# Kernel optimization log

Measured on AMD Instinct MI355X. Metric: run time of the kernel, lower is better.

## Reference

```python
import jax, jax.numpy as jnp
import numpy as np
from jax import lax

TOPK = 5
NUM_CLUSTERS = 10
MAX_ITERS = 10


def setup_inputs() -> dict:
    key = jax.random.key(0)
    k1, k2, k3 = jax.random.split(key, 3)
    B, S, D, K = 8, 4096, 256, 1024
    x = jax.random.normal(k1, (B, S, D), dtype=jnp.float32)
    memory = jax.random.normal(k2, (K, D), dtype=jnp.float32)
    init_idx = jax.random.randint(k3, (B, NUM_CLUSTERS), 0, S, dtype=jnp.int32)
    return {"x": x, "memory": memory, "init_idx": init_idx}


def reference(x, memory, init_idx):
    B, S, D = x.shape
    # --- memory bank retrieval ---
    sim = jnp.einsum('bsd,kd->bsk', x, memory)            # [B,S,K]
    _, topk_idx = lax.top_k(sim, TOPK)                    # [B,S,TOPK]
    memory_ctx = memory[topk_idx]                         # [B,S,TOPK,D]
    attn = jax.nn.softmax(jnp.einsum('bsd,bstd->bst', x, memory_ctx), axis=-1)
    x_enh = x + jnp.einsum('bst,bstd->bsd', attn, memory_ctx)  # [B,S,D]

    # --- in-place k-means ---
    centroids0 = jnp.take_along_axis(x_enh, init_idx[:, :, None], axis=1)  # [B,k,D]
    x_norm_sq = jnp.sum(x_enh ** 2, axis=-1, keepdims=True)                # [B,S,1]

    def step(cent, _):
        dots = jnp.einsum('bsd,bkd->bsk', x_enh, cent)                     # [B,S,k]
        c_norm_sq = jnp.sum(cent ** 2, axis=-1)                            # [B,k]
        dist = x_norm_sq - 2.0 * dots + c_norm_sq[:, None, :]              # [B,S,k]
        assign = jnp.argmin(dist, axis=-1)                                 # [B,S]
        onehot = jax.nn.one_hot(assign, NUM_CLUSTERS, dtype=x_enh.dtype)   # [B,S,k]
        sums = jnp.einsum('bsk,bsd->bkd', onehot, x_enh)                   # [B,k,D]
        counts = jnp.sum(onehot, axis=1)[:, :, None]                       # [B,k,1]
        new_cent = sums / (counts + 1e-8)
        return new_cent, assign

    cent, assigns = lax.scan(step, centroids0, None, length=MAX_ITERS)
    assign = assigns[-1]  # assignments from last iteration (pre final update, as in torch)
    idx = jnp.broadcast_to(assign[:, :, None], (B, S, D))
    quantized = jnp.take_along_axis(cent, idx, axis=1)  # [B,S,D]
    return quantized
```

## Files before the change

kernel.cpp:

```cpp
#include <hip/hip_runtime.h>
#include <math.h>

#define NC 10
#define KITERS 10

#define SWZ(row, q) ((q) ^ (((row) >> 2) & 15))

extern __shared__ float4 lds4[];
__global__ __launch_bounds__(256, 1) void k_enh(const float* __restrict__ x,
                                                const float* __restrict__ mem,
                                                float* __restrict__ xenh) {
  float4* xt = lds4;
  float4* mt = lds4 + 4096;
  float* cv = (float*)lds4;
  int*   ck = (int*)lds4 + 5120;
  float* av = (float*)lds4 + 10240;
  int*   ak = (int*)lds4 + 10560;

  const int tid = threadIdx.x;
  const int tg = tid >> 4;
  const int kg = tid & 15;
  const int tokenBase = blockIdx.x * 64;

  {
    const float4* xg = (const float4*)(x + (size_t)tokenBase * 256);
    const float4* mg = (const float4*)mem;
#pragma unroll
    for (int i = 0; i < 16; ++i) {
      const int p = tid + 256 * i;
      const int row = p >> 6, q = p & 63;
      xt[row * 64 + SWZ(row, q)] = xg[p];
      mt[row * 64 + SWZ(row, q)] = mg[p];
    }
  }
  __syncthreads();

  float t5v[4][5]; int t5k[4][5];
#pragma unroll
  for (int i = 0; i < 4; ++i)
#pragma unroll
    for (int r = 0; r < 5; ++r) { t5v[i][r] = -INFINITY; t5k[i][r] = 0; }

  for (int kc = 0; kc < 16; ++kc) {
    float4 st[16];
    if (kc < 15) {
      const float4* mg = (const float4*)mem + (size_t)(kc + 1) * 4096;
#pragma unroll
      for (int i = 0; i < 16; ++i) st[i] = mg[tid + 256 * i];
    }

    float4 acc[4][4];
#pragma unroll
    for (int i = 0; i < 4; ++i)
#pragma unroll
      for (int j = 0; j < 4; ++j) acc[i][j] = make_float4(0.f, 0.f, 0.f, 0.f);

#pragma unroll 8
    for (int q = 0; q < 64; ++q) {
      float4 mv[4], xv[4];
#pragma unroll
      for (int j = 0; j < 4; ++j) {
        const int row = 4 * kg + j;
        mv[j] = mt[row * 64 + SWZ(row, q)];
      }
#pragma unroll
      for (int i = 0; i < 4; ++i) {
        const int row = 4 * tg + i;
        xv[i] = xt[row * 64 + SWZ(row, q)];
      }
#pragma unroll
      for (int i = 0; i < 4; ++i)
#pragma unroll
        for (int j = 0; j < 4; ++j) {
          acc[i][j].x = __fadd_rn(acc[i][j].x, __fmul_rn(xv[i].x, mv[j].x));
          acc[i][j].y = __fadd_rn(acc[i][j].y, __fmul_rn(xv[i].y, mv[j].y));
          acc[i][j].z = __fadd_rn(acc[i][j].z, __fmul_rn(xv[i].z, mv[j].z));
          acc[i][j].w = __fadd_rn(acc[i][j].w, __fmul_rn(xv[i].w, mv[j].w));
        }
    }

#pragma unroll
    for (int i = 0; i < 4; ++i)
#pragma unroll
      for (int j = 0; j < 4; ++j) {
        const float v = __fadd_rn(__fadd_rn(acc[i][j].x, acc[i][j].z),
                                  __fadd_rn(acc[i][j].y, acc[i][j].w));
        const int kk = kc * 64 + 4 * kg + j;
        if (v > t5v[i][4]) {
          t5v[i][4] = v; t5k[i][4] = kk;
          if (t5v[i][4] > t5v[i][3]) { float a = t5v[i][3]; t5v[i][3] = t5v[i][4]; t5v[i][4] = a; int ia = t5k[i][3]; t5k[i][3] = t5k[i][4]; t5k[i][4] = ia; }
          if (t5v[i][3] > t5v[i][2]) { float a = t5v[i][2]; t5v[i][2] = t5v[i][3]; t5v[i][3] = a; int ia = t5k[i][2]; t5k[i][2] = t5k[i][3]; t5k[i][3] = ia; }
          if (t5v[i][2] > t5v[i][1]) { float a = t5v[i][1]; t5v[i][1] = t5v[i][2]; t5v[i][2] = a; int ia = t5k[i][1]; t5k[i][1] = t5k[i][2]; t5k[i][2] = ia; }
          if (t5v[i][1] > t5v[i][0]) { float a = t5v[i][0]; t5v[i][0] = t5v[i][1]; t5v[i][1] = a; int ia = t5k[i][0]; t5k[i][0] = t5k[i][1]; t5k[i][1] = ia; }
        }
      }

    __syncthreads();
    if (kc < 15) {
#pragma unroll
      for (int i = 0; i < 16; ++i) {
        const int p = tid + 256 * i;
        const int row = p >> 6, q = p & 63;
        mt[row * 64 + SWZ(row, q)] = st[i];
      }
      __syncthreads();
    }
  }
  __syncthreads();

#pragma unroll
  for (int i = 0; i < 4; ++i) {
    const int token = 4 * tg + i;
#pragma unroll
    for (int r = 0; r < 5; ++r) {
      cv[token * 80 + kg * 5 + r] = t5v[i][r];
      ck[token * 80 + kg * 5 + r] = t5k[i][r];
    }
  }
  __syncthreads();

  if (tid < 64) {
    const int token = tid;
    float tv[5]; int tk[5];
#pragma unroll
    for (int r = 0; r < 5; ++r) {
      float best = -INFINITY; int bi = 0, bk = 0x7fffffff;
      for (int c = 0; c < 80; ++c) {
        const float vv = cv[token * 80 + c]; const int kkc = ck[token * 80 + c];
        if (vv > best || (vv == best && kkc < bk)) { best = vv; bi = c; bk = kkc; }
      }
      tv[r] = best; tk[r] = bk; cv[token * 80 + bi] = -INFINITY;
    }
    float mx = tv[0];
#pragma unroll
    for (int r = 1; r < 5; ++r) mx = fmaxf(mx, tv[r]);
    float e[5];
#pragma unroll
    for (int r = 0; r < 5; ++r)
      e[r] = (float)exp((double)__fsub_rn(tv[r], mx));
    float s = e[0];
#pragma unroll
    for (int r = 1; r < 5; ++r) s = __fadd_rn(s, e[r]);
#pragma unroll
    for (int r = 0; r < 5; ++r) { av[token * 5 + r] = __fdiv_rn(e[r], s); ak[token * 5 + r] = tk[r]; }
  }
  __syncthreads();

#pragma unroll
  for (int i = 0; i < 16; ++i) {
    const int flat = tid + 256 * i;
    const int token = flat >> 6, q = flat & 63;
    const float a0 = av[token * 5 + 0], a1 = av[token * 5 + 1], a2 = av[token * 5 + 2],
                a3 = av[token * 5 + 3], a4 = av[token * 5 + 4];
    const float4 xv = ((const float4*)(x + (size_t)(tokenBase + token) * 256))[q];
    const float4 m0 = ((const float4*)(mem + (size_t)ak[token * 5 + 0] * 256))[q];
    const float4 m1 = ((const float4*)(mem + (size_t)ak[token * 5 + 1] * 256))[q];
    const float4 m2 = ((const float4*)(mem + (size_t)ak[token * 5 + 2] * 256))[q];
    const float4 m3 = ((const float4*)(mem + (size_t)ak[token * 5 + 3] * 256))[q];
    const float4 m4 = ((const float4*)(mem + (size_t)ak[token * 5 + 4] * 256))[q];
    float4 o;
    {
      float ctx = __fmul_rn(a0, m0.x);
      ctx = __fadd_rn(ctx, __fmul_rn(a1, m1.x));
      ctx = __fadd_rn(ctx, __fmul_rn(a2, m2.x));
      ctx = __fadd_rn(ctx, __fmul_rn(a3, m3.x));
      ctx = __fadd_rn(ctx, __fmul_rn(a4, m4.x));
      o.x = __fadd_rn(xv.x, ctx);
    }
    {
      float ctx = __fmul_rn(a0, m0.y);
      ctx = __fadd_rn(ctx, __fmul_rn(a1, m1.y));
      ctx = __fadd_rn(ctx, __fmul_rn(a2, m2.y));
      ctx = __fadd_rn(ctx, __fmul_rn(a3, m3.y));
      ctx = __fadd_rn(ctx, __fmul_rn(a4, m4.y));
      o.y = __fadd_rn(xv.y, ctx);
    }
    {
      float ctx = __fmul_rn(a0, m0.z);
      ctx = __fadd_rn(ctx, __fmul_rn(a1, m1.z));
      ctx = __fadd_rn(ctx, __fmul_rn(a2, m2.z));
      ctx = __fadd_rn(ctx, __fmul_rn(a3, m3.z));
      ctx = __fadd_rn(ctx, __fmul_rn(a4, m4.z));
      o.z = __fadd_rn(xv.z, ctx);
    }
    {
      float ctx = __fmul_rn(a0, m0.w);
      ctx = __fadd_rn(ctx, __fmul_rn(a1, m1.w));
      ctx = __fadd_rn(ctx, __fmul_rn(a2, m2.w));
      ctx = __fadd_rn(ctx, __fmul_rn(a3, m3.w));
      ctx = __fadd_rn(ctx, __fmul_rn(a4, m4.w));
      o.w = __fadd_rn(xv.w, ctx);
    }
    ((float4*)(xenh + (size_t)tokenBase * 256))[flat] = o;
  }
}

__global__ __launch_bounds__(256) void k_transpose_x(const float* __restrict__ in,
                                                     float* __restrict__ outT) {
  __shared__ float t[32][33];
  const int tx = threadIdx.x & 31, ty = threadIdx.x >> 5;
  const int s0 = blockIdx.x * 32, d0 = blockIdx.y * 32, b = blockIdx.z;
  const float* ib = in + (size_t)b * 4096 * 256;
  float* ob = outT + (size_t)b * 256 * 4096;
#pragma unroll
  for (int i = 0; i < 4; ++i)
    t[ty + 8 * i][tx] = ib[(size_t)(s0 + ty + 8 * i) * 256 + d0 + tx];
  __syncthreads();
#pragma unroll
  for (int i = 0; i < 4; ++i)
    ob[(size_t)(d0 + ty + 8 * i) * 4096 + s0 + tx] = t[tx][ty + 8 * i];
}

__global__ __launch_bounds__(256) void k_zero(int* __restrict__ p, int n) {
  const int i = blockIdx.x * 256 + threadIdx.x;
  if (i < n) p[i] = 0;
}

__global__ __launch_bounds__(64) void k_init(const float* __restrict__ xenh,
                                             const int* __restrict__ init_idx,
                                             float* __restrict__ cent) {
  const int i = blockIdx.x;
  const int b = i / NC;
  const int s = init_idx[i];
  const int l = threadIdx.x;
  ((float4*)(cent + (size_t)i * 256))[l] =
      ((const float4*)(xenh + ((size_t)b * 4096 + s) * 256))[l];
}

__global__ __launch_bounds__(256) void k_assign(const float* __restrict__ xenh,
                                                const float* __restrict__ cent,
                                                int* __restrict__ assign,
                                                int* __restrict__ cnt) {
  __shared__ float cl[NC * 256];
  const int tid = threadIdx.x;
  const int b = blockIdx.x & 7;
  const int j = blockIdx.x >> 3;
  const int tokenBase = b * 4096 + j * 128;
  for (int i = tid; i < NC * 256; i += 256)
    cl[i] = cent[(size_t)b * NC * 256 + i];
  __syncthreads();

  const int token = tokenBase + (tid >> 1);
  const int h = tid & 1;
  const float4* px4 = (const float4*)(xenh + (size_t)token * 256 + h * 128);
  const float* pc = cl + h * 128;

  float r[NC][8];
  float4 c0 = px4[0], c1 = px4[1];
#pragma unroll
  for (int ib = 0; ib < 16; ++ib) {
    float4 n0, n1;
    if (ib < 15) { n0 = px4[2 * ib + 2]; n1 = px4[2 * ib + 3]; }
    const float p8[8] = {c0.x, c0.y, c0.z, c0.w, c1.x, c1.y, c1.z, c1.w};
    const int i = ib * 8;
    if (ib == 0) {
#pragma unroll
      for (int k = 0; k < NC; ++k)
#pragma unroll
        for (int jj = 0; jj < 8; ++jj) {
          const float d = __fsub_rn(p8[jj], pc[k * 256 + jj]);
          r[k][jj] = __fmul_rn(d, d);
        }
    } else {
#pragma unroll
      for (int k = 0; k < NC; ++k)
#pragma unroll
        for (int jj = 0; jj < 8; ++jj) {
          const float d = __fsub_rn(p8[jj], pc[k * 256 + i + jj]);
          r[k][jj] = __fadd_rn(r[k][jj], __fmul_rn(d, d));
        }
    }
    c0 = n0; c1 = n1;
  }

  float best = INFINITY; int bk = 0;
#pragma unroll
  for (int k = 0; k < NC; ++k) {
    const float blkOwn =
        __fadd_rn(__fadd_rn(__fadd_rn(r[k][0], r[k][1]), __fadd_rn(r[k][2], r[k][3])),
                  __fadd_rn(__fadd_rn(r[k][4], r[k][5]), __fadd_rn(r[k][6], r[k][7])));
    const float blkOther = __shfl_xor(blkOwn, 1);
    const float dist = __fadd_rn(blkOwn, blkOther);
    if (dist < best) { best = dist; bk = k; }
  }
  if (h == 0) assign[token] = bk;
#pragma unroll
  for (int k = 0; k < NC; ++k) {
    const unsigned long long m =
        __ballot(bk == k) & 0x5555555555555555ULL;
    if ((tid & 63) == 0) atomicAdd(&cnt[b * NC + k], (int)__popcll(m));
  }
}

__global__ __launch_bounds__(64) void k_sums_T(const float* __restrict__ xT,
                                               const int* __restrict__ assign,
                                               const int* __restrict__ cnt,
                                               float* __restrict__ cent) {
  const int b = blockIdx.x & 7;
  const int rem = blockIdx.x >> 3;
  const int k = rem >> 2;
  const int d = (rem & 3) * 64 + threadIdx.x;
  const float4* xc = (const float4*)(xT + ((size_t)b * 256 + d) * 4096);
  const int4* ac = (const int4*)(assign + b * 4096);

  float acc = 0.0f;
  for (int c = 0; c < 64; ++c) {
    float4 xe[16]; int4 ar[16];
#pragma unroll
    for (int j = 0; j < 16; ++j) xe[j] = xc[c * 16 + j];
#pragma unroll
    for (int j = 0; j < 16; ++j) ar[j] = ac[c * 16 + j];
#pragma unroll
    for (int j = 0; j < 16; ++j) {
      acc = __fadd_rn(acc, (ar[j].x == k) ? xe[j].x : 0.0f);
      acc = __fadd_rn(acc, (ar[j].y == k) ? xe[j].y : 0.0f);
      acc = __fadd_rn(acc, (ar[j].z == k) ? xe[j].z : 0.0f);
      acc = __fadd_rn(acc, (ar[j].w == k) ? xe[j].w : 0.0f);
    }
  }
  const int cc = cnt[b * NC + k];
  cent[((size_t)(b * NC + k)) * 256 + d] = (cc == 0) ? 0.0f : __fdiv_rn(acc, (float)cc);
}

__global__ __launch_bounds__(64) void k_sums(const float* __restrict__ xenh,
                                             const int* __restrict__ assign,
                                             const int* __restrict__ cnt,
                                             float* __restrict__ cent) {
  const int b = blockIdx.x & 7;
  const int rem = blockIdx.x >> 3;
  const int k = rem >> 2;
  const int d = (rem & 3) * 64 + threadIdx.x;
  const float* xb = xenh + (size_t)b * 4096 * 256 + d;
  const int* ab = assign + b * 4096;

  float acc = 0.0f;
  for (int c = 0; c < 64; ++c) {
    float xe[64]; int ar[64];
#pragma unroll
    for (int j = 0; j < 64; ++j) xe[j] = xb[(size_t)(c * 64 + j) * 256];
#pragma unroll
    for (int j = 0; j < 64; ++j) ar[j] = ab[c * 64 + j];
#pragma unroll
    for (int j = 0; j < 64; ++j)
      acc = __fadd_rn(acc, (ar[j] == k) ? xe[j] : 0.0f);
  }
  const int cc = cnt[b * NC + k];
  cent[((size_t)(b * NC + k)) * 256 + d] = (cc == 0) ? 0.0f : __fdiv_rn(acc, (float)cc);
}

__global__ __launch_bounds__(256) void k_quant(const float* __restrict__ cent,
                                               const int* __restrict__ assign,
                                               float* __restrict__ out) {
  const int token = blockIdx.x * 4 + (threadIdx.x >> 6);
  const int l = threadIdx.x & 63;
  const int b = token >> 12;
  const int a = assign[token];
  ((float4*)out)[(size_t)token * 64 + l] =
      ((const float4*)cent)[(size_t)(b * NC + a) * 64 + l];
}

extern "C" void kernel_launch(void* const* d_in, const int* in_sizes, int n_in,
                              void* d_out, int out_size, void* d_ws, size_t ws_size,
                              hipStream_t stream) {
  const float* x = (const float*)d_in[0];
  const float* mem = (const float*)d_in[1];
  const int* init_idx = (const int*)d_in[2];
  float* xenh = (float*)d_out;
  char* ws = (char*)d_ws;

  float* cent   = (float*)(ws);
  int*   assign = (int*)  (ws + 81920);
  int*   cntbuf = (int*)  (ws + 212992);
  float* xT     = (float*)(ws + (1 << 20));
  const bool useT = ws_size >= ((size_t)34 << 20);

  (void)hipFuncSetAttribute((const void*)k_enh,
                            hipFuncAttributeMaxDynamicSharedMemorySize, 131072);

  k_zero<<<4, 256, 0, stream>>>(cntbuf, KITERS * 8 * NC);
  k_enh<<<512, 256, 131072, stream>>>(x, mem, xenh);
  if (useT) k_transpose_x<<<dim3(128, 8, 8), 256, 0, stream>>>(xenh, xT);
  k_init<<<80, 64, 0, stream>>>(xenh, init_idx, cent);
  for (int it = 0; it < KITERS; ++it) {
    k_assign<<<256, 256, 0, stream>>>(xenh, cent, assign, cntbuf + it * 8 * NC);
    if (useT)
      k_sums_T<<<320, 64, 0, stream>>>(xT, assign, cntbuf + it * 8 * NC, cent);
    else
      k_sums<<<320, 64, 0, stream>>>(xenh, assign, cntbuf + it * 8 * NC, cent);
  }
  k_quant<<<8192, 256, 0, stream>>>(cent, assign, (float*)d_out);
}
```

Baseline: 1.779 ms.

## Stage token tile in padded LDS and split each token across four lanes in assign

The k-means assignment kernel now loads a 64-token tile of x_enh into padded shared memory with coalesced float4 reads, then has four lanes per token compute partial distances that are combined with two shuffles. The grid doubles to 512 blocks and occupancy is set to two blocks per CU. This is meant to raise parallelism and memory coalescing over the old two-lanes-per-token version, which streamed x directly from global memory. In exchange it uses much more LDS per block and issues scalar LDS reads, which may be bank-conflict or LDS-bandwidth bound.

```diff
diff --git a/kernel.cpp b/kernel.cpp
--- a/kernel.cpp
+++ b/kernel.cpp
@@ -7,6 +7,7 @@
 #define SWZ(row, q) ((q) ^ (((row) >> 2) & 15))
 
 extern __shared__ float4 lds4[];
+
 __global__ __launch_bounds__(256, 1) void k_enh(const float* __restrict__ x,
                                                 const float* __restrict__ mem,
                                                 float* __restrict__ xenh) {
@@ -227,67 +228,71 @@
       ((const float4*)(xenh + ((size_t)b * 4096 + s) * 256))[l];
 }
 
-__global__ __launch_bounds__(256) void k_assign(const float* __restrict__ xenh,
-                                                const float* __restrict__ cent,
-                                                int* __restrict__ assign,
-                                                int* __restrict__ cnt) {
-  __shared__ float cl[NC * 256];
+__global__ __launch_bounds__(256, 2) void k_assign(const float* __restrict__ xenh,
+                                                   const float* __restrict__ cent,
+                                                   int* __restrict__ assign,
+                                                   int* __restrict__ cnt) {
+  float* xls = (float*)lds4;
+  float* cl  = (float*)lds4 + 64 * 257;
   const int tid = threadIdx.x;
   const int b = blockIdx.x & 7;
   const int j = blockIdx.x >> 3;
-  const int tokenBase = b * 4096 + j * 128;
+  const int tokenBase = b * 4096 + j * 64;
+
   for (int i = tid; i < NC * 256; i += 256)
     cl[i] = cent[(size_t)b * NC * 256 + i];
-  __syncthreads();
-
-  const int token = tokenBase + (tid >> 1);
-  const int h = tid & 1;
-  const float4* px4 = (const float4*)(xenh + (size_t)token * 256 + h * 128);
-  const float* pc = cl + h * 128;
-
-  float r[NC][8];
-  float4 c0 = px4[0], c1 = px4[1];
-#pragma unroll
-  for (int ib = 0; ib < 16; ++ib) {
-    float4 n0, n1;
-    if (ib < 15) { n0 = px4[2 * ib + 2]; n1 = px4[2 * ib + 3]; }
-    const float p8[8] = {c0.x, c0.y, c0.z, c0.w, c1.x, c1.y, c1.z, c1.w};
-    const int i = ib * 8;
-    if (ib == 0) {
-#pragma unroll
-      for (int k = 0; k < NC; ++k)
-#pragma unroll
-        for (int jj = 0; jj < 8; ++jj) {
-          const float d = __fsub_rn(p8[jj], pc[k * 256 + jj]);
-          r[k][jj] = __fmul_rn(d, d);
-        }
-    } else {
-#pragma unroll
-      for (int k = 0; k < NC; ++k)
-#pragma unroll
-        for (int jj = 0; jj < 8; ++jj) {
-          const float d = __fsub_rn(p8[jj], pc[k * 256 + i + jj]);
-          r[k][jj] = __fadd_rn(r[k][jj], __fmul_rn(d, d));
-        }
-    }
-    c0 = n0; c1 = n1;
-  }
+  {
+    const float4* xg = (const float4*)(xenh + (size_t)tokenBase * 256);
+#pragma unroll
+    for (int i = 0; i < 16; ++i) {
+      const int f = tid + 256 * i;
+      const float4 v = xg[f];
+      const int t = f >> 6, q = f & 63;
+      float* p = xls + t * 257 + 4 * q;
+      p[0] = v.x; p[1] = v.y; p[2] = v.z; p[3] = v.w;
+    }
+  }
+  __syncthreads();
+
+  const int tl = tid >> 2;
+  const int sub = tid & 3;
+  const int h = sub >> 1, jh = sub & 1;
+  const int token = tokenBase + tl;
+  const float* px = xls + tl * 257 + h * 128 + 4 * jh;
+  const float* pc = cl + h * 128 + 4 * jh;
+
+  float r4[NC][4];
+#pragma unroll
+  for (int k = 0; k < NC; ++k)
+#pragma unroll
+    for (int e = 0; e < 4; ++e) {
+      const float d = __fsub_rn(px[e], pc[k * 256 + e]);
+      r4[k][e] = __fmul_rn(d, d);
+    }
+#pragma unroll
+  for (int i = 8; i < 128; i += 8)
+#pragma unroll
+    for (int k = 0; k < NC; ++k)
+#pragma unroll
+      for (int e = 0; e < 4; ++e) {
+        const float d = __fsub_rn(px[i + e], pc[k * 256 + i + e]);
+        r4[k][e] = __fadd_rn(r4[k][e], __fmul_rn(d, d));
+      }
 
   float best = INFINITY; int bk = 0;
 #pragma unroll
   for (int k = 0; k < NC; ++k) {
-    const float blkOwn =
-        __fadd_rn(__fadd_rn(__fadd_rn(r[k][0], r[k][1]), __fadd_rn(r[k][2], r[k][3])),
-                  __fadd_rn(__fadd_rn(r[k][4], r[k][5]), __fadd_rn(r[k][6], r[k][7])));
-    const float blkOther = __shfl_xor(blkOwn, 1);
-    const float dist = __fadd_rn(blkOwn, blkOther);
+    const float halfOwn = __fadd_rn(__fadd_rn(r4[k][0], r4[k][1]),
+                                    __fadd_rn(r4[k][2], r4[k][3]));
+    const float blk = __fadd_rn(halfOwn, __shfl_xor(halfOwn, 1));
+    const float dist = __fadd_rn(blk, __shfl_xor(blk, 2));
     if (dist < best) { best = dist; bk = k; }
   }
-  if (h == 0) assign[token] = bk;
+  if (sub == 0) assign[token] = bk;
 #pragma unroll
   for (int k = 0; k < NC; ++k) {
     const unsigned long long m =
-        __ballot(bk == k) & 0x5555555555555555ULL;
+        __ballot(bk == k) & 0x1111111111111111ULL;
     if ((tid & 63) == 0) atomicAdd(&cnt[b * NC + k], (int)__popcll(m));
   }
 }
@@ -376,13 +381,15 @@
 
   (void)hipFuncSetAttribute((const void*)k_enh,
                             hipFuncAttributeMaxDynamicSharedMemorySize, 131072);
+  (void)hipFuncSetAttribute((const void*)k_assign,
+                            hipFuncAttributeMaxDynamicSharedMemorySize, 76032);
 
   k_zero<<<4, 256, 0, stream>>>(cntbuf, KITERS * 8 * NC);
   k_enh<<<512, 256, 131072, stream>>>(x, mem, xenh);
   if (useT) k_transpose_x<<<dim3(128, 8, 8), 256, 0, stream>>>(xenh, xT);
   k_init<<<80, 64, 0, stream>>>(xenh, init_idx, cent);
   for (int it = 0; it < KITERS; ++it) {
-    k_assign<<<256, 256, 0, stream>>>(xenh, cent, assign, cntbuf + it * 8 * NC);
+    k_assign<<<512, 256, 76032, stream>>>(xenh, cent, assign, cntbuf + it * 8 * NC);
     if (useT)
       k_sums_T<<<320, 64, 0, stream>>>(xT, assign, cntbuf + it * 8 * NC, cent);
     else
```

Measured after the change: 2.213 ms. 1.24x slower.
